# Performance work log

Measured on AMD Instinct MI355X. Metric: run time of the kernel, lower is better.

Reference implementation:

```python
import jax, jax.numpy as jnp
import numpy as np

E, K = 8, 2          # n_experts, top-k
D, O = 768, 3072     # input_size, output_size
B, S = 4, 512        # batch, seq


def setup_inputs() -> dict:
    key = jax.random.key(0)
    k1, k2, k3, k4, k5 = jax.random.split(key, 5)
    x = jax.random.normal(k1, (B, S, D), jnp.float32)
    w_gate = jax.random.normal(k2, (D, E), jnp.float32) * 0.02
    expert_w = jax.random.normal(k3, (E, O, D), jnp.float32) * 0.02
    expert_b = jax.random.normal(k4, (E, O), jnp.float32) * 0.02
    static_w = jax.random.normal(k5, (O, D), jnp.float32) * 0.02
    return {"x": x, "w_gate": w_gate, "expert_w": expert_w,
            "expert_b": expert_b, "static_w": static_w}


def cv_squared(v):
    # torch .var() is unbiased (ddof=1)
    return jnp.var(v, ddof=1) / (jnp.mean(v) ** 2 + 1e-10)


def reference(x, w_gate, expert_w, expert_b, static_w):
    loss_coef = 0.01
    xf = x.reshape(-1, D)                      # [N, D]
    N = xf.shape[0]

    # --- top-k gating (eval path: no noise) ---
    logits = xf @ w_gate                       # [N, E]
    top_v, top_i = jax.lax.top_k(logits, K + 1)
    top_k_gates = jax.nn.softmax(top_v[:, :K], axis=1)   # [N, K]
    gates = jnp.zeros_like(logits).at[
        jnp.arange(N)[:, None], top_i[:, :K]].set(top_k_gates)  # [N, E]

    importance = gates.sum(0)                  # [E]
    load = (gates > 0).sum(0).astype(jnp.float32)
    loss = (cv_squared(importance) + cv_squared(load)) * loss_coef

    # --- experts: F.linear(h, W_e + static_w, b_e), combined by gates ---
    W = expert_w + static_w[None]              # [E, O, D]
    y_e = jnp.einsum('nd,eod->neo', xf, W) + expert_b[None]   # [N, E, O]
    y = jnp.einsum('neo,ne->no', y_e, gates)   # [N, O]

    return y.reshape(B, S, O), loss
```

## Files before the change

kernel.cpp:

```cpp
#include <hip/hip_runtime.h>
#include <hip/hip_bf16.h>
#include <stdint.h>

#define E_ 8
#define D_ 768
#define O_ 3072
#define N_ 2048

typedef __attribute__((ext_vector_type(8))) __bf16 bf16x8;
typedef __attribute__((ext_vector_type(4))) float f32x4;

__device__ __forceinline__ unsigned short f2bf(float f) {
    union { float f; uint32_t u; } a; a.f = f;
    uint32_t u = a.u;
    uint32_t r = (u + 0x7fffu + ((u >> 16) & 1u)) >> 16;
    return (unsigned short)r;
}

__device__ __forceinline__ void async16(const void* g, void* l) {
    __builtin_amdgcn_global_load_lds(
        (const __attribute__((address_space(1))) void*)g,
        (__attribute__((address_space(3))) void*)l, 16, 0, 0);
}

__global__ __launch_bounds__(256) void prologue_kernel(
    const float* __restrict__ x, const float* __restrict__ w_gate,
    const float* __restrict__ ew, const float* __restrict__ sw,
    unsigned short* __restrict__ xb, unsigned short* __restrict__ wb,
    int* __restrict__ choice_e, float* __restrict__ choice_g,
    float* __restrict__ y)
{
    if (blockIdx.x >= 512) {
        int i = (blockIdx.x - 512) * 256 + threadIdx.x;
        int f = i * 4;
        const int od = O_ * D_;
        int e = f / od;
        int rem = f - e * od;
        float4 a = *(const float4*)(ew + f);
        float4 b = *(const float4*)(sw + rem);
        ushort4 o;
        o.x = f2bf(a.x + b.x); o.y = f2bf(a.y + b.y);
        o.z = f2bf(a.z + b.z); o.w = f2bf(a.w + b.w);
        ((ushort4*)wb)[i] = o;
        return;
    }

    int wid  = threadIdx.x >> 6;
    int lane = threadIdx.x & 63;
    int n = blockIdx.x * 4 + wid;
    const float* xr = x + (size_t)n * D_;

    float acc[E_];
#pragma unroll
    for (int e = 0; e < E_; ++e) acc[e] = 0.f;

    for (int c = 0; c < D_ / 64; ++c) {
        int d = c * 64 + lane;
        float xv = xr[d];
        xb[(size_t)n * D_ + d] = f2bf(xv);
        const float* wg = w_gate + (size_t)d * E_;
        float4 w0 = *(const float4*)(wg);
        float4 w1 = *(const float4*)(wg + 4);
        acc[0] += xv * w0.x; acc[1] += xv * w0.y;
        acc[2] += xv * w0.z; acc[3] += xv * w0.w;
        acc[4] += xv * w1.x; acc[5] += xv * w1.y;
        acc[6] += xv * w1.z; acc[7] += xv * w1.w;
    }
#pragma unroll
    for (int e = 0; e < E_; ++e) {
        float v = acc[e];
        for (int off = 32; off > 0; off >>= 1) v += __shfl_xor(v, off, 64);
        acc[e] = v;
    }
    if (lane == 0) {
        int i0 = 0; float v0 = acc[0];
#pragma unroll
        for (int e = 1; e < E_; ++e) if (acc[e] > v0) { v0 = acc[e]; i0 = e; }
        int i1 = -1; float v1 = -3.0e38f;
#pragma unroll
        for (int e = 0; e < E_; ++e) if (e != i0 && acc[e] > v1) { v1 = acc[e]; i1 = e; }
        float ex = expf(v1 - v0);
        float g0 = 1.f / (1.f + ex);
        float g1 = ex / (1.f + ex);
        choice_e[2 * n]     = i0;  choice_g[2 * n]     = g0;
        choice_e[2 * n + 1] = i1;  choice_g[2 * n + 1] = g1;
    }

    float4 z = {0.f, 0.f, 0.f, 0.f};
    float4* yb = (float4*)(y + (size_t)blockIdx.x * 12288);
#pragma unroll
    for (int i = 0; i < 12; ++i) yb[threadIdx.x + 256 * i] = z;
}

__global__ __launch_bounds__(1024) void compact_kernel(
    const int* __restrict__ choice_e, const float* __restrict__ choice_g,
    int* __restrict__ counts, int* __restrict__ pair_token,
    float* __restrict__ pair_gate, float* __restrict__ out_loss)
{
    __shared__ int   s_cnt[E_];
    __shared__ float s_imp[E_];
    int t = threadIdx.x;
    if (t < E_) { s_cnt[t] = 0; s_imp[t] = 0.f; }
    __syncthreads();
    for (int i = t; i < N_ * 2; i += 1024) {
        int e = choice_e[i];
        float gv = choice_g[i];
        int pos = atomicAdd(&s_cnt[e], 1);
        pair_token[e * N_ + pos] = i >> 1;
        pair_gate[e * N_ + pos]  = gv;
        atomicAdd(&s_imp[e], gv);
    }
    __syncthreads();
    if (t < E_) counts[t] = s_cnt[t];
    if (t == 0) {
        float mi = 0.f, ml = 0.f, imp[E_], ld[E_];
#pragma unroll
        for (int i = 0; i < E_; ++i) {
            imp[i] = s_imp[i]; ld[i] = (float)s_cnt[i];
            mi += imp[i]; ml += ld[i];
        }
        mi /= (float)E_; ml /= (float)E_;
        float vi = 0.f, vl = 0.f;
#pragma unroll
        for (int i = 0; i < E_; ++i) {
            vi += (imp[i] - mi) * (imp[i] - mi);
            vl += (ld[i] - ml) * (ld[i] - ml);
        }
        vi /= (float)(E_ - 1); vl /= (float)(E_ - 1);
        *out_loss = 0.01f * (vi / (mi * mi + 1e-10f) + vl / (ml * ml + 1e-10f));
    }
}

#define BM 128
#define BN 128
#define BK 64

__global__ __launch_bounds__(256) void moe_gemm_kernel(
    const unsigned short* __restrict__ xb,
    const unsigned short* __restrict__ wb,
    const float* __restrict__ expert_b,
    const int* __restrict__ counts,
    const int* __restrict__ pair_token,
    const float* __restrict__ pair_gate,
    float* __restrict__ y)
{
    int e = blockIdx.z;
    int cnt = counts[e];
    int m0 = blockIdx.y * BM;
    if (m0 >= cnt) return;
    int n0 = blockIdx.x * BN;

    __shared__ __align__(16) unsigned short sA[BM * BK];
    __shared__ __align__(16) unsigned short sB[BN * BK];

    int tid  = threadIdx.x;
    int lane = tid & 63;
    int wid  = tid >> 6;
    int wm = wid & 1, wn = wid >> 1;
    int l16 = lane & 15;
    int quad = lane >> 4;

    int r0 = tid >> 3;
    int kg = (tid & 7) ^ (r0 & 7);
    const unsigned short* gA[4];
    const unsigned short* gB[4];
#pragma unroll
    for (int s = 0; s < 4; ++s) {
        int row = r0 + 32 * s;
        int ar = m0 + row; if (ar >= cnt) ar = cnt - 1;
        gA[s] = xb + (size_t)pair_token[e * N_ + ar] * D_ + kg * 8;
        gB[s] = wb + ((size_t)e * O_ + n0 + row) * D_ + kg * 8;
    }
    char* lA = (char*)sA + wid * 1024;
    char* lB = (char*)sB + wid * 1024;

    f32x4 acc[4][4];
#pragma unroll
    for (int a = 0; a < 4; ++a)
#pragma unroll
        for (int b = 0; b < 4; ++b) acc[a][b] = (f32x4){0.f, 0.f, 0.f, 0.f};

    for (int k0 = 0; k0 < D_; k0 += BK) {
#pragma unroll
        for (int s = 0; s < 4; ++s) {
            async16(gA[s] + k0, lA + s * 4096);
            async16(gB[s] + k0, lB + s * 4096);
        }
        __syncthreads();

#pragma unroll
        for (int ks = 0; ks < 2; ++ks) {
            bf16x8 af[4], bfr[4];
#pragma unroll
            for (int mi = 0; mi < 4; ++mi) {
                int row = wm * 64 + mi * 16 + l16;
                int ch  = row * 8 + ((ks * 4 + quad) ^ (row & 7));
                af[mi] = *(const bf16x8*)&sA[ch * 8];
            }
#pragma unroll
            for (int ni = 0; ni < 4; ++ni) {
                int row = wn * 64 + ni * 16 + l16;
                int ch  = row * 8 + ((ks * 4 + quad) ^ (row & 7));
                bfr[ni] = *(const bf16x8*)&sB[ch * 8];
            }
#pragma unroll
            for (int mi = 0; mi < 4; ++mi)
#pragma unroll
                for (int ni = 0; ni < 4; ++ni)
                    acc[mi][ni] = __builtin_amdgcn_mfma_f32_16x16x32_bf16(
                        af[mi], bfr[ni], acc[mi][ni], 0, 0, 0);
        }
        __syncthreads();
    }

    float bias[4];
#pragma unroll
    for (int ni = 0; ni < 4; ++ni)
        bias[ni] = expert_b[e * O_ + n0 + wn * 64 + ni * 16 + l16];
#pragma unroll
    for (int mi = 0; mi < 4; ++mi) {
        int rb = m0 + wm * 64 + mi * 16 + quad * 4;
#pragma unroll
        for (int reg = 0; reg < 4; ++reg) {
            int r = rb + reg;
            if (r < cnt) {
                int token  = pair_token[e * N_ + r];
                float gate = pair_gate[e * N_ + r];
#pragma unroll
                for (int ni = 0; ni < 4; ++ni) {
                    int o = n0 + wn * 64 + ni * 16 + l16;
                    atomicAdd(&y[(size_t)token * O_ + o],
                              gate * (acc[mi][ni][reg] + bias[ni]));
                }
            }
        }
    }
}

extern "C" void kernel_launch(void* const* d_in, const int* in_sizes, int n_in,
                              void* d_out, int out_size, void* d_ws, size_t ws_size,
                              hipStream_t stream) {
    const float* x        = (const float*)d_in[0];
    const float* w_gate   = (const float*)d_in[1];
    const float* expert_w = (const float*)d_in[2];
    const float* expert_b = (const float*)d_in[3];
    const float* static_w = (const float*)d_in[4];
    float* out = (float*)d_out;

    char* ws = (char*)d_ws;
    int*   counts     = (int*)(ws + 0);
    int*   pair_token = (int*)(ws + 4096);
    float* pair_gate  = (float*)(ws + 4096 + 65536);
    int*   choice_e   = (int*)(ws + 4096 + 131072);
    float* choice_g   = (float*)(ws + 4096 + 131072 + 16384);
    unsigned short* xb = (unsigned short*)(ws + 4096 + 131072 + 32768);
    unsigned short* wb = (unsigned short*)(ws + 4096 + 131072 + 32768 + 3145728);

    prologue_kernel<<<512 + (E_ * O_ * D_ / 4) / 256, 256, 0, stream>>>(
        x, w_gate, expert_w, static_w, xb, wb, choice_e, choice_g, out);
    compact_kernel<<<1, 1024, 0, stream>>>(choice_e, choice_g, counts,
                                           pair_token, pair_gate, out + (size_t)N_ * O_);

    dim3 grid(O_ / BN, N_ / BM, E_);
    moe_gemm_kernel<<<grid, 256, 0, stream>>>(xb, wb, expert_b, counts,
                                              pair_token, pair_gate, out);
}
```

Measured before the change: 210.2 us.

## Double-buffer GEMM LDS tiles, widen weight conversion, use ballot-based compaction

Result: slower. 215.2 us (+2.4%).

```diff
diff --git a/kernel.cpp b/kernel.cpp
--- a/kernel.cpp
+++ b/kernel.cpp
@@ -32,16 +32,20 @@
 {
     if (blockIdx.x >= 512) {
         int i = (blockIdx.x - 512) * 256 + threadIdx.x;
-        int f = i * 4;
+        int f = i * 8;
         const int od = O_ * D_;
         int e = f / od;
         int rem = f - e * od;
-        float4 a = *(const float4*)(ew + f);
-        float4 b = *(const float4*)(sw + rem);
-        ushort4 o;
-        o.x = f2bf(a.x + b.x); o.y = f2bf(a.y + b.y);
-        o.z = f2bf(a.z + b.z); o.w = f2bf(a.w + b.w);
-        ((ushort4*)wb)[i] = o;
+        float4 a0 = *(const float4*)(ew + f);
+        float4 a1 = *(const float4*)(ew + f + 4);
+        float4 b0 = *(const float4*)(sw + rem);
+        float4 b1 = *(const float4*)(sw + rem + 4);
+        union { ushort u[8]; uint4 v; } o;
+        o.u[0] = f2bf(a0.x + b0.x); o.u[1] = f2bf(a0.y + b0.y);
+        o.u[2] = f2bf(a0.z + b0.z); o.u[3] = f2bf(a0.w + b0.w);
+        o.u[4] = f2bf(a1.x + b1.x); o.u[5] = f2bf(a1.y + b1.y);
+        o.u[6] = f2bf(a1.z + b1.z); o.u[7] = f2bf(a1.w + b1.w);
+        ((uint4*)wb)[i] = o.v;
         return;
     }
 
@@ -100,18 +104,41 @@
     __shared__ int   s_cnt[E_];
     __shared__ float s_imp[E_];
     int t = threadIdx.x;
-    if (t < E_) { s_cnt[t] = 0; s_imp[t] = 0.f; }
+    int lane = t & 63;
+    if (t < E_) s_cnt[t] = 0;
     __syncthreads();
-    for (int i = t; i < N_ * 2; i += 1024) {
-        int e = choice_e[i];
+
+#pragma unroll
+    for (int it = 0; it < (2 * N_) / 1024; ++it) {
+        int i = it * 1024 + t;
+        int ce = choice_e[i];
         float gv = choice_g[i];
-        int pos = atomicAdd(&s_cnt[e], 1);
-        pair_token[e * N_ + pos] = i >> 1;
-        pair_gate[e * N_ + pos]  = gv;
-        atomicAdd(&s_imp[e], gv);
+        unsigned long long mask[E_];
+#pragma unroll
+        for (int e = 0; e < E_; ++e) mask[e] = __ballot(ce == e);
+        int b = 0;
+        if (lane < E_) b = atomicAdd(&s_cnt[lane], __popcll(mask[lane]));
+        int mybase = __shfl(b, ce, 64);
+        unsigned long long mymask = mask[0];
+#pragma unroll
+        for (int e = 1; e < E_; ++e) if (ce == e) mymask = mask[e];
+        int pos = mybase + __popcll(mymask & ((1ull << lane) - 1ull));
+        pair_token[ce * N_ + pos] = i >> 1;
+        pair_gate[ce * N_ + pos]  = gv;
     }
     __syncthreads();
     if (t < E_) counts[t] = s_cnt[t];
+
+    if (t < 256) {
+        int e = t >> 5, l = t & 31;
+        int cnt = s_cnt[e];
+        float p = 0.f;
+        for (int i = l; i < cnt; i += 32) p += pair_gate[e * N_ + i];
+#pragma unroll
+        for (int off = 16; off > 0; off >>= 1) p += __shfl_down(p, off, 32);
+        if (l == 0) s_imp[e] = p;
+    }
+    __syncthreads();
     if (t == 0) {
         float mi = 0.f, ml = 0.f, imp[E_], ld[E_];
 #pragma unroll
@@ -150,8 +177,8 @@
     if (m0 >= cnt) return;
     int n0 = blockIdx.x * BN;
 
-    __shared__ __align__(16) unsigned short sA[BM * BK];
-    __shared__ __align__(16) unsigned short sB[BN * BK];
+    __shared__ __align__(16) unsigned short sA[2][BM * BK];
+    __shared__ __align__(16) unsigned short sB[2][BN * BK];
 
     int tid  = threadIdx.x;
     int lane = tid & 63;
@@ -171,8 +198,8 @@
         gA[s] = xb + (size_t)pair_token[e * N_ + ar] * D_ + kg * 8;
         gB[s] = wb + ((size_t)e * O_ + n0 + row) * D_ + kg * 8;
     }
-    char* lA = (char*)sA + wid * 1024;
-    char* lB = (char*)sB + wid * 1024;
+    char* lA[2] = { (char*)sA[0] + wid * 1024, (char*)sA[1] + wid * 1024 };
+    char* lB[2] = { (char*)sB[0] + wid * 1024, (char*)sB[1] + wid * 1024 };
 
     f32x4 acc[4][4];
 #pragma unroll
@@ -180,14 +207,23 @@
 #pragma unroll
         for (int b = 0; b < 4; ++b) acc[a][b] = (f32x4){0.f, 0.f, 0.f, 0.f};
 
-    for (int k0 = 0; k0 < D_; k0 += BK) {
-#pragma unroll
-        for (int s = 0; s < 4; ++s) {
-            async16(gA[s] + k0, lA + s * 4096);
-            async16(gB[s] + k0, lB + s * 4096);
-        }
+#pragma unroll
+    for (int s = 0; s < 4; ++s) {
+        async16(gA[s], lA[0] + s * 4096);
+        async16(gB[s], lB[0] + s * 4096);
+    }
+
+    int kb = 0;
+    for (int k0 = 0; k0 < D_; k0 += BK, kb ^= 1) {
         __syncthreads();
-
+        int kn = k0 + BK;
+        if (kn < D_) {
+#pragma unroll
+            for (int s = 0; s < 4; ++s) {
+                async16(gA[s] + kn, lA[kb ^ 1] + s * 4096);
+                async16(gB[s] + kn, lB[kb ^ 1] + s * 4096);
+            }
+        }
 #pragma unroll
         for (int ks = 0; ks < 2; ++ks) {
             bf16x8 af[4], bfr[4];
@@ -195,13 +231,13 @@
             for (int mi = 0; mi < 4; ++mi) {
                 int row = wm * 64 + mi * 16 + l16;
                 int ch  = row * 8 + ((ks * 4 + quad) ^ (row & 7));
-                af[mi] = *(const bf16x8*)&sA[ch * 8];
+                af[mi] = *(const bf16x8*)&sA[kb][ch * 8];
             }
 #pragma unroll
             for (int ni = 0; ni < 4; ++ni) {
                 int row = wn * 64 + ni * 16 + l16;
                 int ch  = row * 8 + ((ks * 4 + quad) ^ (row & 7));
-                bfr[ni] = *(const bf16x8*)&sB[ch * 8];
+                bfr[ni] = *(const bf16x8*)&sB[kb][ch * 8];
             }
 #pragma unroll
             for (int mi = 0; mi < 4; ++mi)
@@ -210,7 +246,6 @@
                     acc[mi][ni] = __builtin_amdgcn_mfma_f32_16x16x32_bf16(
                         af[mi], bfr[ni], acc[mi][ni], 0, 0, 0);
         }
-        __syncthreads();
     }
 
     float bias[4];
@@ -256,7 +291,7 @@
     unsigned short* xb = (unsigned short*)(ws + 4096 + 131072 + 32768);
     unsigned short* wb = (unsigned short*)(ws + 4096 + 131072 + 32768 + 3145728);
 
-    prologue_kernel<<<512 + (E_ * O_ * D_ / 4) / 256, 256, 0, stream>>>(
+    prologue_kernel<<<512 + (E_ * O_ * D_ / 8) / 256, 256, 0, stream>>>(
         x, w_gate, expert_w, static_w, xb, wb, choice_e, choice_g, out);
     compact_kernel<<<1, 1024, 0, stream>>>(choice_e, choice_g, counts,
                                            pair_token, pair_gate, out + (size_t)N_ * O_);
```
